# Kernel tuning notes

Hardware: AMD Instinct MI355X
Metric: run time of the kernel (lower is better)

## Reference

```python
import jax, jax.numpy as jnp
import numpy as np

N_EDGES = 6000
NUM_IMGS = 5  # 1 reference + 4 source views
H = W = 800
NUM_HALF_V = 10  # hardcoded in sample_points_2d


def setup_inputs() -> dict:
    rng = np.random.default_rng(0)
    # 3D edge endpoints in camera space, in front of the camera
    start = rng.normal(0.0, 0.3, (N_EDGES, 3)).astype(np.float32)
    start[:, 2] += 2.5
    d = rng.normal(size=(N_EDGES, 3))
    d /= np.linalg.norm(d, axis=1, keepdims=True)
    length = rng.uniform(0.3, 0.7, (N_EDGES, 1))
    end = (start + d * length).astype(np.float32)
    # num_horizontal = clamp(norm/0.01, 2, 1000) -- integer, no gradient, so
    # the ragged coordinate template is precomputed here (faithful to torch)
    num_h = np.clip((np.linalg.norm(end - start, axis=-1) / 0.01).astype(np.int64), 2, 1000)
    edge_idx_x = np.repeat(np.arange(N_EDGES), num_h)
    begin = np.concatenate(([0], np.cumsum(num_h)[:-1]))
    dx = (np.arange(num_h.sum()) - begin[edge_idx_x]) / (num_h - 1)[edge_idx_x]
    dy = np.arange(NUM_HALF_V) / (NUM_HALF_V - 1)
    dy = np.concatenate((-dy[::-1], dy))  # [20]
    coords_x = np.repeat(dx, 2 * NUM_HALF_V).astype(np.float32)  # [T]
    coords_y = np.tile(dy, int(num_h.sum())).astype(np.float32)  # [T]
    edge_idx = np.repeat(edge_idx_x, 2 * NUM_HALF_V).astype(np.int64)  # [T]
    num_per_edge = (num_h * NUM_HALF_V * 2).astype(np.int64)  # [N]
    imgs = rng.random((NUM_IMGS, H, W)).astype(np.float32)
    intrinsic = np.array([[0.8, 0.0, 0.5], [0.0, 0.8, 0.5], [0.0, 0.0, 1.0]], dtype=np.float32)
    trans = np.zeros((NUM_IMGS - 1, 3, 4), dtype=np.float32)
    for i in range(NUM_IMGS - 1):
        Rt = np.eye(3, 4, dtype=np.float32)
        Rt[:, 3] = rng.normal(0.0, 0.05, 3)
        trans[i] = intrinsic @ Rt
    return {
        'start_points': jnp.asarray(start),
        'end_points': jnp.asarray(end),
        'imgs': jnp.asarray(imgs),
        'transformations': jnp.asarray(trans),
        'intrinsic': jnp.asarray(intrinsic),
        'coords_x': jnp.asarray(coords_x),
        'coords_y': jnp.asarray(coords_y),
        'edge_idx': jnp.asarray(edge_idx),
        'num_per_edge': jnp.asarray(num_per_edge),
    }


def _bilinear(img, uv):
    # img [H,W], uv [T,2] in [0,1); grid_sample(align_corners=False) convention
    Hh, Ww = img.shape
    x = uv[:, 0] * Ww - 0.5
    y = uv[:, 1] * Hh - 0.5
    x0 = jnp.floor(x)
    y0 = jnp.floor(y)
    wx = x - x0
    wy = y - y0
    x0i = jnp.clip(x0.astype(jnp.int32), 0, Ww - 1)
    x1i = jnp.clip(x0i + 1, 0, Ww - 1)
    y0i = jnp.clip(y0.astype(jnp.int32), 0, Hh - 1)
    y1i = jnp.clip(y0i + 1, 0, Hh - 1)
    v00 = img[y0i, x0i]
    v01 = img[y0i, x1i]
    v10 = img[y1i, x0i]
    v11 = img[y1i, x1i]
    return (v00 * (1 - wx) + v01 * wx) * (1 - wy) + (v10 * (1 - wx) + v11 * wx) * wy


def reference(start_points, end_points, imgs, transformations, intrinsic,
              coords_x, coords_y, edge_idx, num_per_edge):
    num_src = imgs.shape[0] - 1
    img_w = imgs.shape[2]
    n_edges = start_points.shape[0]
    # interleave endpoints: [2N,3]
    points_c = jnp.stack([start_points, end_points], axis=1).reshape(-1, 3)

    def sample_template(ep):
        # ep: [N,2,2] projected 2D edge endpoints -> per-coordinate 2D points [T,2]
        p0 = ep[:, 0]
        cur_dir = ep[:, 1] - ep[:, 0]
        dir3 = jnp.concatenate([cur_dir, jnp.zeros_like(cur_dir[:, :1])], axis=1)
        z = jnp.zeros_like(dir3).at[:, 2].set(1.0)
        c = jnp.cross(dir3, z)[:, :2]
        edge_up = c / (jnp.linalg.norm(c, axis=-1, keepdims=True) + 1e-6) * (10.0 / img_w)
        return (cur_dir[edge_idx] * coords_x[:, None]
                + edge_up[edge_idx] * coords_y[:, None]
                + p0[edge_idx])

    # reference view projection (pinhole, normalized coords)
    proj = (intrinsic @ points_c.T).T
    ep1 = (proj[:, :2] / (proj[:, 2:3] + 1e-6)).reshape(-1, 2, 2)
    p2d1 = sample_template(ep1)  # [T,2]
    vm1 = jnp.all((p2d1 > 0) & (p2d1 < 1), axis=-1)
    p2d1 = jnp.clip(p2d1, 0.0, 0.999999)

    # source view projections
    hom = jnp.concatenate([points_c, jnp.ones_like(points_c[:, :1])], axis=1)  # [2N,4]
    projs = jnp.einsum('sij,nj->sni', transformations, hom)
    ep2 = (projs[..., :2] / (projs[..., 2:3] + 1e-6)).reshape(num_src, -1, 2, 2)
    p2d2 = jax.vmap(sample_template)(ep2)  # [S,T,2]
    vm2 = jnp.all((p2d2 > 0) & (p2d2 < 1), axis=-1)
    p2d2 = jnp.clip(p2d2, 0.0, 0.999999)

    # bilinear image sampling (irregular gather)
    s1 = _bilinear(imgs[0], p2d1)  # [T]
    s2 = jax.vmap(_bilinear)(imgs[1:], p2d2)  # [S,T]

    # loss4: per-edge mean squared photometric difference; black-area detection
    cnt = num_per_edge.astype(jnp.float32)
    seg_sum = lambda v: jax.ops.segment_sum(v, edge_idx, num_segments=n_edges)
    diff2 = (s2 - s1[None, :]) ** 2  # [S,T]
    similarity_loss = jax.vmap(seg_sum)(diff2) / cnt[None, :]  # [S,N]
    black_area = (seg_sum((s1 < 0.01).astype(jnp.float32)) / cnt) > 0.5  # [N]

    # scatter_min of per-point validity -> per-edge mask
    sim_mask_pts = (vm1[None, :] & vm2).astype(jnp.int32)  # [S,T]
    seg_min = lambda m: jax.ops.segment_min(m, edge_idx, num_segments=n_edges)
    similarity_mask = jax.vmap(seg_min)(sim_mask_pts).astype(bool)  # [S,N]

    return similarity_loss, similarity_mask, black_area, p2d1, p2d2
```

## Files before the change

### kernel.cpp

```cpp
#include <hip/hip_runtime.h>
#include <math.h>

#define IMG_W   800
#define IMG_PIX (IMG_W * IMG_W)
#define NEDGE   6000
#define NSRC    4
#define NVIEW   5
#define HDR (2 * NSRC * NEDGE + NEDGE)

typedef float vf4 __attribute__((ext_vector_type(4)));

struct __attribute__((packed, aligned(4))) f2u { float a, b; };

__device__ __forceinline__ f2u ld2(const float* __restrict__ p) {
    return *(const f2u*)p;
}
__device__ __forceinline__ void st4(float* p, float a, float b, float c, float d,
                                    bool nt) {
    vf4 v; v.x = a; v.y = b; v.z = c; v.w = d;
    if (nt) __builtin_nontemporal_store(v, (vf4*)p);
    else    *(vf4*)p = v;
}

__global__ void __launch_bounds__(256)
points_kernel(const float* __restrict__ sp,
              const float* __restrict__ epnt,
              const float* __restrict__ K,
              const float* __restrict__ T,
              const int* __restrict__ npe,
              const float* __restrict__ imgs,
              float* __restrict__ out,
              int P) {
    const int e = blockIdx.x;
    const int nsamp = npe[e];
    const int nh = nsamp / 20;
    const int t = threadIdx.x;
    const int lane = t & 63, wid = t >> 6;

    __shared__ float DX[1000];
    __shared__ float DY[20];
    __shared__ float rS[4][5];
    __shared__ int   rM[4];
    __shared__ int   redI[4];

    for (int h = t; h < nh; h += 256)
        DX[h] = (float)((double)h / (double)(nh - 1));
    if (t < 20)
        DY[t] = (t < 10) ? -(float)((double)(9 - t) / 9.0)
                         :  (float)((double)(t - 10) / 9.0);

    int partial = 0;
    for (int i = t; i < e; i += 256) partial += npe[i];
#pragma unroll
    for (int off = 32; off > 0; off >>= 1)
        partial += __shfl_down(partial, off);
    if (lane == 0) redI[wid] = partial;
    __syncthreads();
    const int b20 = redI[0] + redI[1] + redI[2] + redI[3];

    float Ax[NVIEW], Ay[NVIEW], Az[NVIEW], Aw[NVIEW], Bx[NVIEW], By[NVIEW];
    {
        float sx = sp[3 * e], sy = sp[3 * e + 1], sz = sp[3 * e + 2];
        float ex = epnt[3 * e], ey = epnt[3 * e + 1], ez = epnt[3 * e + 2];
#pragma unroll
        for (int v = 0; v < NVIEW; ++v) {
            float as, bs, cs, ae, be, ce;
            if (v == 0) {
                as = K[0] * sx + K[1] * sy + K[2] * sz;
                bs = K[3] * sx + K[4] * sy + K[5] * sz;
                cs = K[6] * sx + K[7] * sy + K[8] * sz;
                ae = K[0] * ex + K[1] * ey + K[2] * ez;
                be = K[3] * ex + K[4] * ey + K[5] * ez;
                ce = K[6] * ex + K[7] * ey + K[8] * ez;
            } else {
                const float* tt = T + (v - 1) * 12;
                as = tt[0] * sx + tt[1] * sy + tt[2] * sz + tt[3];
                bs = tt[4] * sx + tt[5] * sy + tt[6] * sz + tt[7];
                cs = tt[8] * sx + tt[9] * sy + tt[10] * sz + tt[11];
                ae = tt[0] * ex + tt[1] * ey + tt[2] * ez + tt[3];
                be = tt[4] * ex + tt[5] * ey + tt[6] * ez + tt[7];
                ce = tt[8] * ex + tt[9] * ey + tt[10] * ez + tt[11];
            }
            float u0 = as / (cs + 1e-6f);
            float w0 = bs / (cs + 1e-6f);
            float u1 = ae / (ce + 1e-6f);
            float w1 = be / (ce + 1e-6f);
            float dx = u1 - u0, dy = w1 - w0;
            float cxx = dy, cyy = -dx;
            float nrm = sqrtf(cxx * cxx + cyy * cyy);
            float inv = 1.f / (nrm + 1e-6f) * (10.0f / (float)IMG_W);
            Ax[v] = u0; Ay[v] = w0; Az[v] = dx; Aw[v] = dy;
            Bx[v] = cxx * inv; By[v] = cyy * inv;
        }
    }

    float* vbase[NVIEW];
    bool   val64[NVIEW];
    {
        size_t gb = (size_t)b20;
        vbase[0] = out + HDR + 2 * gb;
#pragma unroll
        for (int s = 0; s < NSRC; ++s)
            vbase[s + 1] = out + HDR + 2 * (size_t)P + 2 * ((size_t)s * P + gb);
#pragma unroll
        for (int v = 0; v < NVIEW; ++v)
            val64[v] = ((((size_t)vbase[v]) & 63) == 0);
    }

    float accs[NSRC] = {0.f, 0.f, 0.f, 0.f};
    float accB = 0.f;
    unsigned maskAcc = 0x1Fu;

    for (int base = 0; base < nsamp; base += 1024) {
        int q0 = base + 2 * t;
        int q1 = base + 512 + 2 * t;
        bool v0 = (q0 < nsamp);
        bool v1 = (q1 < nsamp);

        float px[4 * NVIEW], py[4 * NVIEW];
#pragma unroll
        for (int k = 0; k < 4; ++k) {
            bool ok = (k < 2) ? v0 : v1;
            if (!ok) continue;
            int p = ((k < 2) ? q0 : q1) + (k & 1);
            int h = p / 20;
            int m = p - h * 20;
            float xk = DX[h];
            float yk = DY[m];
            unsigned mb = 0;
#pragma unroll
            for (int v = 0; v < NVIEW; ++v) {
                float ux = Az[v] * xk + Bx[v] * yk + Ax[v];
                float uy = Aw[v] * xk + By[v] * yk + Ay[v];
                if ((ux > 0.f) && (ux < 1.f) && (uy > 0.f) && (uy < 1.f))
                    mb |= (1u << v);
                px[k * NVIEW + v] = fminf(fmaxf(ux, 0.f), 0.999999f);
                py[k * NVIEW + v] = fminf(fmaxf(uy, 0.f), 0.999999f);
            }
            maskAcc &= mb;
        }

#pragma unroll
        for (int v = 0; v < NVIEW; ++v) {
            float* bp = vbase[v] + 2 * base;
            if (v0) st4(bp + 4 * t,
                        px[0 * NVIEW + v], py[0 * NVIEW + v],
                        px[1 * NVIEW + v], py[1 * NVIEW + v], val64[v]);
            if (v1) st4(bp + 1024 + 4 * t,
                        px[2 * NVIEW + v], py[2 * NVIEW + v],
                        px[3 * NVIEW + v], py[3 * NVIEW + v], val64[v]);
        }

        f2u r0[4 * NVIEW], r1[4 * NVIEW];
        unsigned hib = 0;
#pragma unroll
        for (int k = 0; k < 4; ++k) {
            bool ok = (k < 2) ? v0 : v1;
            if (!ok) continue;
#pragma unroll
            for (int v = 0; v < NVIEW; ++v) {
                int j = k * NVIEW + v;
                float fx = px[j] * (float)IMG_W - 0.5f;
                float fy = py[j] * (float)IMG_W - 0.5f;
                float xf = floorf(fx), yf = floorf(fy);
                px[j] = fx - xf;
                py[j] = fy - yf;
                int x0 = (int)xf;
                int y0 = (int)yf;
                int xc = min(max(x0, 0), IMG_W - 2);
                int y0i = min(max(y0, 0), IMG_W - 1);
                int y1i = min(y0i + 1, IMG_W - 1);
                if (x0 >= IMG_W - 1) hib |= (1u << j);
                const float* im = imgs + v * IMG_PIX;
                r0[j] = ld2(im + y0i * IMG_W + xc);
                r1[j] = ld2(im + y1i * IMG_W + xc);
            }
        }
#pragma unroll
        for (int k = 0; k < 4; ++k) {
            bool ok = (k < 2) ? v0 : v1;
            if (!ok) continue;
            float sval[NVIEW];
#pragma unroll
            for (int v = 0; v < NVIEW; ++v) {
                int j = k * NVIEW + v;
                bool hi = (hib >> j) & 1u;
                float v00 = hi ? r0[j].b : r0[j].a;
                float v01 = r0[j].b;
                float v10 = hi ? r1[j].b : r1[j].a;
                float v11 = r1[j].b;
                float wxv = px[j], wyv = py[j];
                sval[v] = (v00 * (1.f - wxv) + v01 * wxv) * (1.f - wyv)
                        + (v10 * (1.f - wxv) + v11 * wxv) * wyv;
            }
            float s1 = sval[0];
            accB += (s1 < 0.01f) ? 1.f : 0.f;
#pragma unroll
            for (int s = 0; s < NSRC; ++s) {
                float d = sval[s + 1] - s1;
                accs[s] += d * d;
            }
        }
    }

    int mi = (int)maskAcc;
#pragma unroll
    for (int off = 32; off > 0; off >>= 1) {
        accs[0] += __shfl_down(accs[0], off);
        accs[1] += __shfl_down(accs[1], off);
        accs[2] += __shfl_down(accs[2], off);
        accs[3] += __shfl_down(accs[3], off);
        accB    += __shfl_down(accB, off);
        mi      &= __shfl_down(mi, off);
    }
    if (lane == 0) {
        rS[wid][0] = accs[0]; rS[wid][1] = accs[1];
        rS[wid][2] = accs[2]; rS[wid][3] = accs[3];
        rS[wid][4] = accB;
        rM[wid] = mi;
    }
    __syncthreads();
    if (t == 0) {
        float s0 = 0.f, s1 = 0.f, s2 = 0.f, s3 = 0.f, sB = 0.f;
        int m = 0x1F;
#pragma unroll
        for (int w = 0; w < 4; ++w) {
            s0 += rS[w][0]; s1 += rS[w][1]; s2 += rS[w][2]; s3 += rS[w][3];
            sB += rS[w][4];
            m  &= rM[w];
        }
        float cnt = (float)nsamp;
        out[0 * NEDGE + e] = s0 / cnt;
        out[1 * NEDGE + e] = s1 / cnt;
        out[2 * NEDGE + e] = s2 / cnt;
        out[3 * NEDGE + e] = s3 / cnt;
        bool vm1 = m & 1;
#pragma unroll
        for (int s = 0; s < NSRC; ++s)
            out[NSRC * NEDGE + s * NEDGE + e] =
                (vm1 && ((m >> (s + 1)) & 1)) ? 1.f : 0.f;
        out[2 * NSRC * NEDGE + e] = ((sB / cnt) > 0.5f) ? 1.f : 0.f;
    }
}

extern "C" void kernel_launch(void* const* d_in, const int* in_sizes, int n_in,
                              void* d_out, int out_size, void* d_ws, size_t ws_size,
                              hipStream_t stream) {
    const float* start = (const float*)d_in[0];
    const float* endp  = (const float*)d_in[1];
    const float* imgs  = (const float*)d_in[2];
    const float* trans = (const float*)d_in[3];
    const float* K     = (const float*)d_in[4];
    const int*   npe   = (const int*)d_in[8];
    int P = in_sizes[5];

    float* out = (float*)d_out;
    points_kernel<<<NEDGE, 256, 0, stream>>>(start, endp, K, trans, npe, imgs,
                                             out, P);
}
```

Baseline: 415.1 us.

## Precompute edge offsets with a separate prefix-scan kernel

```diff
diff --git a/kernel.cpp b/kernel.cpp
--- a/kernel.cpp
+++ b/kernel.cpp
@@ -9,17 +9,48 @@
 #define HDR (2 * NSRC * NEDGE + NEDGE)
 
 typedef float vf4 __attribute__((ext_vector_type(4)));
-
-struct __attribute__((packed, aligned(4))) f2u { float a, b; };
-
-__device__ __forceinline__ f2u ld2(const float* __restrict__ p) {
-    return *(const f2u*)p;
+typedef float vf2 __attribute__((ext_vector_type(2)));
+typedef vf2 uvf2 __attribute__((aligned(4)));
+
+__device__ __forceinline__ vf2 ld2(const float* __restrict__ p) {
+    return *(const uvf2*)p;
 }
 __device__ __forceinline__ void st4(float* p, float a, float b, float c, float d,
                                     bool nt) {
     vf4 v; v.x = a; v.y = b; v.z = c; v.w = d;
     if (nt) __builtin_nontemporal_store(v, (vf4*)p);
     else    *(vf4*)p = v;
+}
+
+__global__ void __launch_bounds__(256)
+scan_kernel(const int* __restrict__ npe, int* __restrict__ bg) {
+    __shared__ int part[256];
+    int t = threadIdx.x;
+    int base = t * 24;
+    int loc[24];
+    int s = 0;
+#pragma unroll
+    for (int i = 0; i < 24; ++i) {
+        int idx = base + i;
+        int v = (idx < NEDGE) ? npe[idx] : 0;
+        loc[i] = s;
+        s += v;
+    }
+    part[t] = s;
+    __syncthreads();
+    int own = s;
+    for (int off = 1; off < 256; off <<= 1) {
+        int v = (t >= off) ? part[t - off] : 0;
+        __syncthreads();
+        part[t] += v;
+        __syncthreads();
+    }
+    int myoff = part[t] - own;
+#pragma unroll
+    for (int i = 0; i < 24; ++i) {
+        int idx = base + i;
+        if (idx < NEDGE) bg[idx] = myoff + loc[i];
+    }
 }
 
 __global__ void __launch_bounds__(256)
@@ -28,12 +59,14 @@
               const float* __restrict__ K,
               const float* __restrict__ T,
               const int* __restrict__ npe,
+              const int* __restrict__ bg,
               const float* __restrict__ imgs,
               float* __restrict__ out,
               int P) {
     const int e = blockIdx.x;
     const int nsamp = npe[e];
     const int nh = nsamp / 20;
+    const int b20 = bg[e];
     const int t = threadIdx.x;
     const int lane = t & 63, wid = t >> 6;
 
@@ -41,22 +74,12 @@
     __shared__ float DY[20];
     __shared__ float rS[4][5];
     __shared__ int   rM[4];
-    __shared__ int   redI[4];
 
     for (int h = t; h < nh; h += 256)
         DX[h] = (float)((double)h / (double)(nh - 1));
     if (t < 20)
         DY[t] = (t < 10) ? -(float)((double)(9 - t) / 9.0)
                          :  (float)((double)(t - 10) / 9.0);
-
-    int partial = 0;
-    for (int i = t; i < e; i += 256) partial += npe[i];
-#pragma unroll
-    for (int off = 32; off > 0; off >>= 1)
-        partial += __shfl_down(partial, off);
-    if (lane == 0) redI[wid] = partial;
-    __syncthreads();
-    const int b20 = redI[0] + redI[1] + redI[2] + redI[3];
 
     float Ax[NVIEW], Ay[NVIEW], Az[NVIEW], Aw[NVIEW], Bx[NVIEW], By[NVIEW];
     {
@@ -106,6 +129,7 @@
         for (int v = 0; v < NVIEW; ++v)
             val64[v] = ((((size_t)vbase[v]) & 63) == 0);
     }
+    __syncthreads();
 
     float accs[NSRC] = {0.f, 0.f, 0.f, 0.f};
     float accB = 0.f;
@@ -151,7 +175,7 @@
                         px[3 * NVIEW + v], py[3 * NVIEW + v], val64[v]);
         }
 
-        f2u r0[4 * NVIEW], r1[4 * NVIEW];
+        vf2 r0[4 * NVIEW], r1[4 * NVIEW];
         unsigned hib = 0;
 #pragma unroll
         for (int k = 0; k < 4; ++k) {
@@ -185,10 +209,10 @@
             for (int v = 0; v < NVIEW; ++v) {
                 int j = k * NVIEW + v;
                 bool hi = (hib >> j) & 1u;
-                float v00 = hi ? r0[j].b : r0[j].a;
-                float v01 = r0[j].b;
-                float v10 = hi ? r1[j].b : r1[j].a;
-                float v11 = r1[j].b;
+                float v00 = hi ? r0[j].y : r0[j].x;
+                float v01 = r0[j].y;
+                float v10 = hi ? r1[j].y : r1[j].x;
+                float v11 = r1[j].y;
                 float wxv = px[j], wyv = py[j];
                 sval[v] = (v00 * (1.f - wxv) + v01 * wxv) * (1.f - wyv)
                         + (v10 * (1.f - wxv) + v11 * wxv) * wyv;
@@ -254,7 +278,10 @@
     const int*   npe   = (const int*)d_in[8];
     int P = in_sizes[5];
 
+    int* bg = (int*)d_ws;
+
     float* out = (float*)d_out;
-    points_kernel<<<NEDGE, 256, 0, stream>>>(start, endp, K, trans, npe, imgs,
-                                             out, P);
-}
+    scan_kernel<<<1, 256, 0, stream>>>(npe, bg);
+    points_kernel<<<NEDGE, 256, 0, stream>>>(start, endp, K, trans, npe, bg,
+                                             imgs, out, P);
+}
```

New measurement: 399.8 us. 1.04x faster.
